# Optimization experiments

Measured on AMD Instinct MI355X. Metric: run time of the kernel, lower is better.

## Reference

```python
import jax, jax.numpy as jnp
import numpy as np

B, L, V, D = 8, 1024, 64, 64  # num_vars == d_model required by the module's g*h broadcast
EPS = 1e-5


def _layer_norm(x, gamma, beta):
    mu = jnp.mean(x, axis=-1, keepdims=True)
    var = jnp.mean(jnp.square(x - mu), axis=-1, keepdims=True)
    return (x - mu) * jax.lax.rsqrt(var + EPS) * gamma + beta


def setup_inputs() -> dict:
    key = jax.random.key(0)
    ks = jax.random.split(key, 20)
    s = 0.05
    inp = {
        'x': jax.random.normal(ks[0], (B, L, V), jnp.float32),
        # per-variable GRN(1, D, D) params, batched over V
        'W1': jax.random.normal(ks[1], (V, D), jnp.float32) * s,   # lin1 weight [in=1 -> D]
        'b1': jax.random.normal(ks[2], (V, D), jnp.float32) * s,
        'W2': jax.random.normal(ks[3], (V, D, D), jnp.float32) * s,
        'b2': jax.random.normal(ks[4], (V, D), jnp.float32) * s,
        'Wg': jax.random.normal(ks[5], (V, D, D), jnp.float32) * s,
        'bg': jax.random.normal(ks[6], (V, D), jnp.float32) * s,
        'Wsk': jax.random.normal(ks[7], (V, D), jnp.float32) * s,  # skip Linear(1, D)
        'bsk': jax.random.normal(ks[8], (V, D), jnp.float32) * s,
        'gamma': jnp.ones((V, D), jnp.float32),
        'beta': jnp.zeros((V, D), jnp.float32),
        # weight_net GRN(V*D, D, V) params
        'Wn1': jax.random.normal(ks[9], (V * D, D), jnp.float32) * s,
        'bn1': jax.random.normal(ks[10], (D,), jnp.float32) * s,
        'Wn2': jax.random.normal(ks[11], (D, D), jnp.float32) * s,
        'bn2': jax.random.normal(ks[12], (D,), jnp.float32) * s,
        'Wng': jax.random.normal(ks[13], (D, V), jnp.float32) * s,
        'bng': jax.random.normal(ks[14], (V,), jnp.float32) * s,
        'Wns': jax.random.normal(ks[15], (V * D, V), jnp.float32) * s,
        'bns': jax.random.normal(ks[16], (V,), jnp.float32) * s,
        'ngamma': jnp.ones((V,), jnp.float32),
        'nbeta': jnp.zeros((V,), jnp.float32),
    }
    return inp


def reference(x, W1, b1, W2, b2, Wg, bg, Wsk, bsk, gamma, beta,
              Wn1, bn1, Wn2, bn2, Wng, bng, Wns, bns, ngamma, nbeta):
    Bx, Lx, Vx = x.shape
    # --- per-variable GRN(1, D, D), batched over the variable axis ---
    h1 = jax.nn.elu(x[..., None] * W1 + b1)                      # [B,L,V,D]
    h2 = jnp.einsum('blvd,vde->blve', h1, W2) + b2               # [B,L,V,D]
    g = jax.nn.sigmoid(jnp.einsum('blvd,vde->blve', h2, Wg) + bg)
    skip = x[..., None] * Wsk + bsk                              # [B,L,V,D]
    stacked = _layer_norm(skip + g * h2, gamma, beta)            # [B,L,V,D]
    # --- weight net GRN(V*D, D, V) + softmax (note: requires V == D) ---
    flat = stacked.reshape(Bx, Lx, Vx * stacked.shape[-1])
    hw = jax.nn.elu(flat @ Wn1 + bn1)                            # [B,L,D]
    hw = hw @ Wn2 + bn2                                          # [B,L,D]
    gw = jax.nn.sigmoid(hw @ Wng + bng)                          # [B,L,V]
    skw = flat @ Wns + bns                                       # [B,L,V]
    weights = jax.nn.softmax(_layer_norm(skw + gw * hw, ngamma, nbeta), axis=-1)
    return jnp.einsum('blv,blvd->bld', weights, stacked)
```

## Files before the change

kernel.cpp:

```cpp
#include <hip/hip_runtime.h>
#include <hip/hip_bf16.h>
#include <math.h>

#define NV 64
#define ND 64
#define NTOK 8192
#define LN_EPS 1e-5f
#define SROW 4096
#define WROW 4096
#define KSPLIT 8
#define KR2 (4096 / KSPLIT)
#define BK 64
#define NKC (KR2 / BK)
#define PROW2 (KSPLIT * 128)

typedef __attribute__((ext_vector_type(8))) short s8v;
typedef __attribute__((ext_vector_type(4))) float f4v;
typedef __attribute__((ext_vector_type(4))) int   i4v;

__device__ __forceinline__ float sigm_f(float x) {
    return __builtin_amdgcn_rcpf(1.f + __expf(-x));
}
__device__ __forceinline__ float elu_f(float x)  { return x > 0.f ? x : (__expf(x) - 1.f); }

__device__ __forceinline__ float bf16_to_f(unsigned short s) {
    union { unsigned int u; float f; } c; c.u = ((unsigned int)s) << 16;
    return c.f;
}
__device__ __forceinline__ unsigned short bf16_rn(float f) {
    union { float f; unsigned int u; } c; c.f = f;
    return (unsigned short)((c.u + 0x8000u) >> 16);
}
__device__ __forceinline__ void async16(const void* g, void* l) {
    __builtin_amdgcn_global_load_lds(
        (const __attribute__((address_space(1))) unsigned int*)g,
        (__attribute__((address_space(3))) unsigned int*)l,
        16, 0, 0);
}

__global__ __launch_bounds__(256) void vsn_prepack(
    const float* __restrict__ W2, const float* __restrict__ Wg,
    const float* __restrict__ Wn1, const float* __restrict__ Wns,
    short* __restrict__ w2b, short* __restrict__ wgb,
    short* __restrict__ wct)
{
    __shared__ float T[64][65];
    const int b = blockIdx.x, t = threadIdx.x;

    if (b < 64) {
        const float* src = W2 + (size_t)b * 4096;
        short* dst = w2b + (size_t)b * 4096;
        #pragma unroll
        for (int pass = 0; pass < 2; ++pass) {
            #pragma unroll
            for (int i = 0; i < 16; ++i) {
                int id = i * 256 + t;
                T[id & 63][id >> 6] = src[id];
            }
            __syncthreads();
            #pragma unroll
            for (int i = 0; i < 16; ++i) {
                int id = i * 256 + t;
                dst[id] = (short)bf16_rn(T[id >> 6][id & 63]);
            }
            __syncthreads();
            src = Wg + (size_t)b * 4096;
            dst = wgb + (size_t)b * 4096;
        }
    } else {
        int tb = b - 64;
        int half = tb >> 6, kt = tb & 63;
        const float* src = (half == 0 ? Wn1 : Wns) + (size_t)(kt * 64) * 64;
        #pragma unroll
        for (int i = 0; i < 16; ++i) {
            int id = i * 256 + t;
            T[id & 63][id >> 6] = src[id];
        }
        __syncthreads();
        #pragma unroll
        for (int i = 0; i < 16; ++i) {
            int id = i * 256 + t;
            int n = id >> 6, r = id & 63;
            wct[(size_t)(half * 64 + n) * WROW + kt * 64 + r] = (short)bf16_rn(T[n][r]);
        }
    }
}

__global__ __launch_bounds__(256) void vsn_stage1(
    const float* __restrict__ x,
    const float* __restrict__ W1, const float* __restrict__ b1,
    const short* __restrict__ w2b, const short* __restrict__ wgb,
    const float* __restrict__ b2, const float* __restrict__ bg,
    const float* __restrict__ Wsk, const float* __restrict__ bsk,
    const float* __restrict__ gamma, const float* __restrict__ beta,
    unsigned short* __restrict__ stb)
{
    const int t = threadIdx.x;
    const int wave = t >> 6, lane = t & 63;
    const int m16 = lane & 15, quad = lane >> 4;
    const int v = blockIdx.y * 4 + wave;

    __shared__ float xs[4][32];
    __shared__ __align__(16) unsigned short h2s[4][32][72];

    float w1k[2][8], b1k[2][8];
    #pragma unroll
    for (int kt = 0; kt < 2; ++kt) {
        *(float4*)&w1k[kt][0] = *(const float4*)(W1 + v * 64 + kt * 32 + quad * 8);
        *(float4*)&w1k[kt][4] = *(const float4*)(W1 + v * 64 + kt * 32 + quad * 8 + 4);
        *(float4*)&b1k[kt][0] = *(const float4*)(b1 + v * 64 + kt * 32 + quad * 8);
        *(float4*)&b1k[kt][4] = *(const float4*)(b1 + v * 64 + kt * 32 + quad * 8 + 4);
    }
    float b2d[4], bgd[4], wskd[4], bskd[4], gamd[4], betd[4];
    #pragma unroll
    for (int ni = 0; ni < 4; ++ni) {
        int d = v * 64 + ni * 16 + m16;
        b2d[ni] = b2[d]; bgd[ni] = bg[d]; wskd[ni] = Wsk[d]; bskd[ni] = bsk[d];
        gamd[ni] = gamma[d]; betd[ni] = beta[d];
    }
    const size_t wb = (size_t)v * 4096;

    for (int tt4 = 0; tt4 < 4; ++tt4) {
        const int tile0 = blockIdx.x * 128 + tt4 * 32;

        if (lane < 32) xs[wave][lane] = x[(size_t)(tile0 + lane) * NV + v];

        s8v a[2][2];
        #pragma unroll
        for (int kt = 0; kt < 2; ++kt)
            #pragma unroll
            for (int mi = 0; mi < 2; ++mi) {
                float xv = xs[wave][mi * 16 + m16];
                float h[8];
                #pragma unroll
                for (int j = 0; j < 8; ++j) h[j] = elu_f(fmaf(xv, w1k[kt][j], b1k[kt][j]));
                i4v av;
                #pragma unroll
                for (int p = 0; p < 4; ++p) {
                    unsigned int u0 = __float_as_uint(h[2 * p]);
                    unsigned int u1 = __float_as_uint(h[2 * p + 1]);
                    av[p] = (int)((u1 & 0xffff0000u) | (u0 >> 16));
                }
                a[mi][kt] = *(s8v*)&av;
            }

        f4v hacc[2][4];
        #pragma unroll
        for (int mi = 0; mi < 2; ++mi)
            #pragma unroll
            for (int ni = 0; ni < 4; ++ni) hacc[mi][ni] = (f4v){0.f, 0.f, 0.f, 0.f};
        #pragma unroll
        for (int ni = 0; ni < 4; ++ni)
            #pragma unroll
            for (int kt = 0; kt < 2; ++kt) {
                s8v bh = *(const s8v*)(w2b + wb + (size_t)(ni * 16 + m16) * 64 + kt * 32 + quad * 8);
                #pragma unroll
                for (int mi = 0; mi < 2; ++mi)
                    hacc[mi][ni] = __builtin_amdgcn_mfma_f32_16x16x32_bf16(a[mi][kt], bh, hacc[mi][ni], 0, 0, 0);
            }
        #pragma unroll
        for (int mi = 0; mi < 2; ++mi)
            #pragma unroll
            for (int ni = 0; ni < 4; ++ni)
                #pragma unroll
                for (int r = 0; r < 4; ++r) hacc[mi][ni][r] += b2d[ni];

        #pragma unroll
        for (int mi = 0; mi < 2; ++mi)
            #pragma unroll
            for (int ni = 0; ni < 4; ++ni)
                #pragma unroll
                for (int r = 0; r < 4; ++r)
                    h2s[wave][mi * 16 + quad * 4 + r][ni * 16 + m16] =
                        (unsigned short)(__float_as_uint(hacc[mi][ni][r]) >> 16);

        s8v c[2][2];
        #pragma unroll
        for (int mi = 0; mi < 2; ++mi)
            #pragma unroll
            for (int kt = 0; kt < 2; ++kt)
                c[mi][kt] = *(const s8v*)&h2s[wave][mi * 16 + m16][kt * 32 + quad * 8];

        f4v gacc[2][4];
        #pragma unroll
        for (int mi = 0; mi < 2; ++mi)
            #pragma unroll
            for (int ni = 0; ni < 4; ++ni) gacc[mi][ni] = (f4v){0.f, 0.f, 0.f, 0.f};
        #pragma unroll
        for (int ni = 0; ni < 4; ++ni)
            #pragma unroll
            for (int kt = 0; kt < 2; ++kt) {
                s8v bh = *(const s8v*)(wgb + wb + (size_t)(ni * 16 + m16) * 64 + kt * 32 + quad * 8);
                #pragma unroll
                for (int mi = 0; mi < 2; ++mi)
                    gacc[mi][ni] = __builtin_amdgcn_mfma_f32_16x16x32_bf16(c[mi][kt], bh, gacc[mi][ni], 0, 0, 0);
            }

        {
            float xtok[2][4];
            #pragma unroll
            for (int mi = 0; mi < 2; ++mi)
                #pragma unroll
                for (int r = 0; r < 4; ++r) xtok[mi][r] = xs[wave][mi * 16 + quad * 4 + r];
            #pragma unroll
            for (int mi = 0; mi < 2; ++mi)
                #pragma unroll
                for (int ni = 0; ni < 4; ++ni)
                    #pragma unroll
                    for (int r = 0; r < 4; ++r) {
                        float g = sigm_f(gacc[mi][ni][r] + bgd[ni]);
                        gacc[mi][ni][r] = fmaf(xtok[mi][r], wskd[ni], bskd[ni]) + g * hacc[mi][ni][r];
                    }
        }

        #pragma unroll
        for (int mi = 0; mi < 2; ++mi)
            #pragma unroll
            for (int r = 0; r < 4; ++r) {
                float s0 = gacc[mi][0][r], s1 = gacc[mi][1][r], s2 = gacc[mi][2][r], s3 = gacc[mi][3][r];
                float sum = s0 + s1 + s2 + s3;
                float sq  = s0 * s0 + s1 * s1 + s2 * s2 + s3 * s3;
                #pragma unroll
                for (int m = 1; m < 16; m <<= 1) { sum += __shfl_xor(sum, m); sq += __shfl_xor(sq, m); }
                float mu  = sum * 0.015625f;
                float var = sq * 0.015625f - mu * mu;
                float rs  = __builtin_amdgcn_rsqf(var + LN_EPS);
                size_t base = (size_t)(tile0 + mi * 16 + quad * 4 + r) * SROW + (size_t)v * 64 + m16;
                #pragma unroll
                for (int ni = 0; ni < 4; ++ni)
                    stb[base + ni * 16] =
                        bf16_rn((gacc[mi][ni][r] - mu) * rs * gamd[ni] + betd[ni]);
            }
    }
}

__global__ __launch_bounds__(512) void vsn_stage2a(
    const unsigned short* __restrict__ stb,
    const short* __restrict__ wct,
    float* __restrict__ part)
{
    const int t = threadIdx.x;
    const int wave = t >> 6, lane = t & 63;
    const int m16 = lane & 15, quad = lane >> 4;
    const int mw = wave & 3, nw = wave >> 2;
    const int tok0 = blockIdx.x * 128;
    const int s = blockIdx.y;
    const int k0 = s * KR2;

    __shared__ __align__(16) unsigned short Al[2][128 * 64];
    __shared__ __align__(16) unsigned short Bl[2][128 * 64];

    const int srow = t >> 3;
    const int schunk = t & 7;

    f4v acc[2][4];
    #pragma unroll
    for (int mi = 0; mi < 2; ++mi)
        #pragma unroll
        for (int nj = 0; nj < 4; ++nj) acc[mi][nj] = (f4v){0.f, 0.f, 0.f, 0.f};

    auto STAGE = [&](int buf, int kc) {
        const int kb = k0 + kc * BK;
        #pragma unroll
        for (int q = 0; q < 2; ++q) {
            const int row = srow + q * 64;
            const int sc = (schunk ^ (row & 7)) * 8;
            async16(stb + (size_t)(tok0 + row) * SROW + kb + sc,
                    &Al[buf][q * 4096 + wave * 512]);
            async16(wct + (size_t)row * WROW + kb + sc,
                    &Bl[buf][q * 4096 + wave * 512]);
        }
    };

    STAGE(0, 0);
    STAGE(1, 1);

    for (int kc = 0; kc < NKC; ++kc) {
        const int buf = kc & 1;
        if (kc + 1 < NKC) asm volatile("s_waitcnt vmcnt(4)" ::: "memory");
        else              asm volatile("s_waitcnt vmcnt(0)" ::: "memory");
        __builtin_amdgcn_s_barrier();
        __builtin_amdgcn_sched_barrier(0);

        #pragma unroll
        for (int ks = 0; ks < 2; ++ks) {
            s8v af[2], bfr[4];
            #pragma unroll
            for (int mi = 0; mi < 2; ++mi) {
                int row = mw * 32 + mi * 16 + m16;
                int ch = ((ks * 4 + quad) ^ (row & 7)) * 8;
                af[mi] = *(const s8v*)&Al[buf][row * 64 + ch];
            }
            #pragma unroll
            for (int nj = 0; nj < 4; ++nj) {
                int row = nw * 64 + nj * 16 + m16;
                int ch = ((ks * 4 + quad) ^ (row & 7)) * 8;
                bfr[nj] = *(const s8v*)&Bl[buf][row * 64 + ch];
            }
            #pragma unroll
            for (int mi = 0; mi < 2; ++mi)
                #pragma unroll
                for (int nj = 0; nj < 4; ++nj)
                    acc[mi][nj] = __builtin_amdgcn_mfma_f32_16x16x32_bf16(af[mi], bfr[nj], acc[mi][nj], 0, 0, 0);
        }

        asm volatile("s_waitcnt lgkmcnt(0)" ::: "memory");
        __builtin_amdgcn_s_barrier();
        __builtin_amdgcn_sched_barrier(0);
        if (kc + 2 < NKC) STAGE(buf, kc + 2);
    }

    #pragma unroll
    for (int mi = 0; mi < 2; ++mi)
        #pragma unroll
        for (int nj = 0; nj < 4; ++nj)
            #pragma unroll
            for (int r = 0; r < 4; ++r)
                part[(size_t)(tok0 + mw * 32 + mi * 16 + quad * 4 + r) * PROW2
                     + s * 128 + nw * 64 + nj * 16 + m16] = acc[mi][nj][r];
}

__global__ __launch_bounds__(256) void vsn_stage2b(
    const unsigned short* __restrict__ stb, const float* __restrict__ part,
    const float* __restrict__ bn1,
    const float* __restrict__ Wn2, const float* __restrict__ bn2,
    const float* __restrict__ Wng, const float* __restrict__ bng,
    const float* __restrict__ bns,
    const float* __restrict__ ngamma, const float* __restrict__ nbeta,
    float* __restrict__ out)
{
    const int t = threadIdx.x;
    const int tok0 = blockIdx.x * 8;
    const int lane = t & 63, wv = t >> 6;

    __shared__ __align__(16) float hw1_s[8][64];
    __shared__ __align__(16) float skw_s[8][64];
    __shared__ __align__(16) float hw2_s[8][64];
    __shared__ float s2_s[8][64];
    __shared__ float w_s[8][64];

    #pragma unroll
    for (int tk = 0; tk < 2; ++tk) {
        int tl = wv * 2 + tk;
        const float* pr = part + (size_t)(tok0 + tl) * PROW2
                        + (lane >> 5) * 128 + (lane & 31) * 4;
        float tv[4] = {0.f, 0.f, 0.f, 0.f};
        #pragma unroll
        for (int i = 0; i < 4; ++i) {
            float4 a = *(const float4*)(pr + i * 256);
            tv[0] += a.x; tv[1] += a.y; tv[2] += a.z; tv[3] += a.w;
        }
        #pragma unroll
        for (int c = 0; c < 4; ++c) tv[c] += __shfl_xor(tv[c], 32);
        if (lane < 16) {
            int j0 = lane * 4;
            float4 bb = *(const float4*)(bn1 + j0);
            hw1_s[tl][j0 + 0] = elu_f(tv[0] + bb.x);
            hw1_s[tl][j0 + 1] = elu_f(tv[1] + bb.y);
            hw1_s[tl][j0 + 2] = elu_f(tv[2] + bb.z);
            hw1_s[tl][j0 + 3] = elu_f(tv[3] + bb.w);
        } else if (lane < 32) {
            int j0 = (lane - 16) * 4;
            float4 bb = *(const float4*)(bns + j0);
            skw_s[tl][j0 + 0] = tv[0] + bb.x;
            skw_s[tl][j0 + 1] = tv[1] + bb.y;
            skw_s[tl][j0 + 2] = tv[2] + bb.z;
            skw_s[tl][j0 + 3] = tv[3] + bb.w;
        }
    }
    __syncthreads();

    #pragma unroll
    for (int i = 0; i < 2; ++i) {
        int oidx = i * 256 + t;
        int tt = oidx >> 6, jj = oidx & 63;
        float acc = bn2[jj];
        #pragma unroll
        for (int k4 = 0; k4 < 16; ++k4) {
            float4 h = *(const float4*)&hw1_s[tt][k4 * 4];
            acc += h.x * Wn2[(k4*4+0)*64+jj] + h.y * Wn2[(k4*4+1)*64+jj]
                 + h.z * Wn2[(k4*4+2)*64+jj] + h.w * Wn2[(k4*4+3)*64+jj];
        }
        hw2_s[tt][jj] = acc;
    }
    __syncthreads();

    #pragma unroll
    for (int i = 0; i < 2; ++i) {
        int oidx = i * 256 + t;
        int tt = oidx >> 6, vv = oidx & 63;
        float acc = bng[vv];
        #pragma unroll
        for (int k4 = 0; k4 < 16; ++k4) {
            float4 h = *(const float4*)&hw2_s[tt][k4 * 4];
            acc += h.x * Wng[(k4*4+0)*64+vv] + h.y * Wng[(k4*4+1)*64+vv]
                 + h.z * Wng[(k4*4+2)*64+vv] + h.w * Wng[(k4*4+3)*64+vv];
        }
        float gw = sigm_f(acc);
        s2_s[tt][vv] = skw_s[tt][vv] + gw * hw2_s[tt][vv];
    }
    __syncthreads();

    const int vloc = lane >> 3, d8 = (lane & 7) * 8;
    s8v r0[8], r1[8];
    {
        const short* s0 = (const short*)stb + (size_t)(tok0 + wv * 2) * SROW + d8;
        const short* s1 = s0 + SROW;
        #pragma unroll
        for (int vc = 0; vc < 8; ++vc) {
            r0[vc] = *(const s8v*)(s0 + (vc * 8 + vloc) * 64);
            r1[vc] = *(const s8v*)(s1 + (vc * 8 + vloc) * 64);
        }
    }

    if (t < 128) {
        int tt = t >> 4, l = t & 15;
        float z[4]; float sum = 0.f, sq = 0.f;
        #pragma unroll
        for (int i = 0; i < 4; ++i) { z[i] = s2_s[tt][l + 16 * i]; sum += z[i]; sq += z[i] * z[i]; }
        #pragma unroll
        for (int m = 1; m < 16; m <<= 1) { sum += __shfl_xor(sum, m); sq += __shfl_xor(sq, m); }
        float mu  = sum * 0.015625f;
        float var = sq * 0.015625f - mu * mu;
        float rs  = __builtin_amdgcn_rsqf(var + LN_EPS);
        float ln[4]; float mx = -1e30f;
        #pragma unroll
        for (int i = 0; i < 4; ++i) {
            ln[i] = (z[i] - mu) * rs * ngamma[l + 16 * i] + nbeta[l + 16 * i];
            mx = fmaxf(mx, ln[i]);
        }
        #pragma unroll
        for (int m = 1; m < 16; m <<= 1) mx = fmaxf(mx, __shfl_xor(mx, m));
        float es = 0.f; float ev[4];
        #pragma unroll
        for (int i = 0; i < 4; ++i) { ev[i] = __expf(ln[i] - mx); es += ev[i]; }
        #pragma unroll
        for (int m = 1; m < 16; m <<= 1) es += __shfl_xor(es, m);
        float inv = __builtin_amdgcn_rcpf(es);
        #pragma unroll
        for (int i = 0; i < 4; ++i) w_s[tt][l + 16 * i] = ev[i] * inv;
    }
    __syncthreads();

    {
        float acc0[8], acc1[8];
        #pragma unroll
        for (int j = 0; j < 8; ++j) { acc0[j] = 0.f; acc1[j] = 0.f; }
        #pragma unroll
        for (int vc = 0; vc < 8; ++vc) {
            int v = vc * 8 + vloc;
            float w0 = w_s[wv * 2][v], w1 = w_s[wv * 2 + 1][v];
            #pragma unroll
            for (int j = 0; j < 8; ++j) {
                acc0[j] = fmaf(w0, bf16_to_f((unsigned short)r0[vc][j]), acc0[j]);
                acc1[j] = fmaf(w1, bf16_to_f((unsigned short)r1[vc][j]), acc1[j]);
            }
        }
        #pragma unroll
        for (int m = 8; m <= 32; m <<= 1)
            #pragma unroll
            for (int j = 0; j < 8; ++j) {
                acc0[j] += __shfl_xor(acc0[j], m);
                acc1[j] += __shfl_xor(acc1[j], m);
            }
        if (lane < 8) {
            float* op = out + (size_t)(tok0 + wv * 2) * 64 + lane * 8;
            *(float4*)op       = make_float4(acc0[0], acc0[1], acc0[2], acc0[3]);
            *(float4*)(op + 4) = make_float4(acc0[4], acc0[5], acc0[6], acc0[7]);
            op += 64;
            *(float4*)op       = make_float4(acc1[0], acc1[1], acc1[2], acc1[3]);
            *(float4*)(op + 4) = make_float4(acc1[4], acc1[5], acc1[6], acc1[7]);
        }
    }
}

extern "C" void kernel_launch(void* const* d_in, const int* in_sizes, int n_in,
                              void* d_out, int out_size, void* d_ws, size_t ws_size,
                              hipStream_t stream) {
    const float* x     = (const float*)d_in[0];
    const float* W1    = (const float*)d_in[1];
    const float* b1    = (const float*)d_in[2];
    const float* W2    = (const float*)d_in[3];
    const float* b2    = (const float*)d_in[4];
    const float* Wg    = (const float*)d_in[5];
    const float* bg    = (const float*)d_in[6];
    const float* Wsk   = (const float*)d_in[7];
    const float* bsk   = (const float*)d_in[8];
    const float* gamma = (const float*)d_in[9];
    const float* beta  = (const float*)d_in[10];
    const float* Wn1   = (const float*)d_in[11];
    const float* bn1   = (const float*)d_in[12];
    const float* Wn2   = (const float*)d_in[13];
    const float* bn2   = (const float*)d_in[14];
    const float* Wng   = (const float*)d_in[15];
    const float* bng   = (const float*)d_in[16];
    const float* Wns   = (const float*)d_in[17];
    const float* bns   = (const float*)d_in[18];
    const float* ngam  = (const float*)d_in[19];
    const float* nbet  = (const float*)d_in[20];

    char* ws = (char*)d_ws;
    unsigned short* stb = (unsigned short*)ws;
    short* wct = (short*)(ws + (64u << 20));
    short* w2b = (short*)(ws + (65u << 20));
    short* wgb = w2b + 262144;
    float* part = (float*)(ws + (66u << 20));
    float* outp = (float*)d_out;

    vsn_prepack<<<dim3(192), 256, 0, stream>>>(W2, Wg, Wn1, Wns, w2b, wgb, wct);
    vsn_stage1<<<dim3(NTOK / 128, 16), 256, 0, stream>>>(
        x, W1, b1, w2b, wgb, b2, bg, Wsk, bsk, gamma, beta, stb);
    vsn_stage2a<<<dim3(NTOK / 128, KSPLIT), 512, 0, stream>>>(stb, wct, part);
    vsn_stage2b<<<dim3(NTOK / 8), 256, 0, stream>>>(
        stb, part, bn1, Wn2, bn2, Wng, bng, bns, ngam, nbet, outp);
}
```

Measured before the change: 185.5 us.

## Fuse weight-net GEMM and epilogue into one kernel without split-K partials

Replaces the split-K stage2a GEMM and the separate stage2b epilogue with a single kernel. Each block handles 32 tokens over the full 4096-wide K, keeps the 128 output columns in registers, and then runs the ELU, Wn2/Wng matvecs, layer norm, softmax and weighted sum in shared memory. This removes the fp32 partial-sum buffer round trip and one launch. Wn2 and Wng are pre-transposed in the prepack kernel so their reads are contiguous. The trade-off is fewer blocks (256) each running a long serial K loop with little MFMA work per wave, and every block re-streams the whole 1 MB wct matrix.

After: 240.2 us. 29.5% more time.

```diff
diff --git a/kernel.cpp b/kernel.cpp
--- a/kernel.cpp
+++ b/kernel.cpp
@@ -8,11 +8,9 @@
 #define LN_EPS 1e-5f
 #define SROW 4096
 #define WROW 4096
-#define KSPLIT 8
-#define KR2 (4096 / KSPLIT)
 #define BK 64
-#define NKC (KR2 / BK)
-#define PROW2 (KSPLIT * 128)
+#define NKC2 (4096 / BK)
+#define MT 32
 
 typedef __attribute__((ext_vector_type(8))) short s8v;
 typedef __attribute__((ext_vector_type(4))) float f4v;
@@ -41,8 +39,10 @@
 __global__ __launch_bounds__(256) void vsn_prepack(
     const float* __restrict__ W2, const float* __restrict__ Wg,
     const float* __restrict__ Wn1, const float* __restrict__ Wns,
+    const float* __restrict__ Wn2, const float* __restrict__ Wng,
     short* __restrict__ w2b, short* __restrict__ wgb,
-    short* __restrict__ wct)
+    short* __restrict__ wct,
+    float* __restrict__ Wn2T, float* __restrict__ WngT)
 {
     __shared__ float T[64][65];
     const int b = blockIdx.x, t = threadIdx.x;
@@ -67,7 +67,7 @@
             src = Wg + (size_t)b * 4096;
             dst = wgb + (size_t)b * 4096;
         }
-    } else {
+    } else if (b < 192) {
         int tb = b - 64;
         int half = tb >> 6, kt = tb & 63;
         const float* src = (half == 0 ? Wn1 : Wns) + (size_t)(kt * 64) * 64;
@@ -82,6 +82,20 @@
             int id = i * 256 + t;
             int n = id >> 6, r = id & 63;
             wct[(size_t)(half * 64 + n) * WROW + kt * 64 + r] = (short)bf16_rn(T[n][r]);
+        }
+    } else {
+        const float* src = (b == 192 ? Wn2 : Wng);
+        float* dst = (b == 192 ? Wn2T : WngT);
+        #pragma unroll
+        for (int i = 0; i < 16; ++i) {
+            int id = i * 256 + t;
+            T[id & 63][id >> 6] = src[id];
+        }
+        __syncthreads();
+        #pragma unroll
+        for (int i = 0; i < 16; ++i) {
+            int id = i * 256 + t;
+            dst[id] = T[id >> 6][id & 63];
         }
     }
 }
@@ -234,190 +248,143 @@
     }
 }
 
-__global__ __launch_bounds__(512) void vsn_stage2a(
+__global__ __launch_bounds__(512) void vsn_stage2(
     const unsigned short* __restrict__ stb,
     const short* __restrict__ wct,
-    float* __restrict__ part)
+    const float* __restrict__ Wn2T, const float* __restrict__ WngT,
+    const float* __restrict__ bn1, const float* __restrict__ bn2,
+    const float* __restrict__ bng, const float* __restrict__ bns,
+    const float* __restrict__ ngamma, const float* __restrict__ nbeta,
+    float* __restrict__ out)
 {
     const int t = threadIdx.x;
     const int wave = t >> 6, lane = t & 63;
     const int m16 = lane & 15, quad = lane >> 4;
-    const int mw = wave & 3, nw = wave >> 2;
-    const int tok0 = blockIdx.x * 128;
-    const int s = blockIdx.y;
-    const int k0 = s * KR2;
-
-    __shared__ __align__(16) unsigned short Al[2][128 * 64];
-    __shared__ __align__(16) unsigned short Bl[2][128 * 64];
-
-    const int srow = t >> 3;
-    const int schunk = t & 7;
-
-    f4v acc[2][4];
-    #pragma unroll
-    for (int mi = 0; mi < 2; ++mi)
-        #pragma unroll
-        for (int nj = 0; nj < 4; ++nj) acc[mi][nj] = (f4v){0.f, 0.f, 0.f, 0.f};
+    const int tok0 = blockIdx.x * MT;
+
+    __shared__ __align__(16) unsigned char smem[43520];
+    unsigned short* Al0 = (unsigned short*)smem;
+    unsigned short* Bl0 = (unsigned short*)(smem + 8192);
+    float* hw1_s = (float*)smem;
+    float* skw_s = (float*)(smem + 8704);
+    float* hw2_s = (float*)(smem + 17408);
+    float* s2_s  = (float*)(smem + 26112);
+    float* w_s   = (float*)(smem + 34816);
+
+    f4v acc[2];
+    acc[0] = (f4v){0.f, 0.f, 0.f, 0.f};
+    acc[1] = (f4v){0.f, 0.f, 0.f, 0.f};
 
     auto STAGE = [&](int buf, int kc) {
-        const int kb = k0 + kc * BK;
+        const int kb = kc * BK;
         #pragma unroll
         for (int q = 0; q < 2; ++q) {
-            const int row = srow + q * 64;
-            const int sc = (schunk ^ (row & 7)) * 8;
+            const int row = wave * 16 + q * 8 + (lane >> 3);
+            const int sc = ((lane & 7) ^ (row & 7)) * 8;
+            async16(wct + (size_t)row * WROW + kb + sc,
+                    &Bl0[buf * 8192 + wave * 1024 + q * 512]);
+        }
+        if (wave < 4) {
+            const int row = wave * 8 + (lane >> 3);
+            const int sc = ((lane & 7) ^ (row & 7)) * 8;
             async16(stb + (size_t)(tok0 + row) * SROW + kb + sc,
-                    &Al[buf][q * 4096 + wave * 512]);
-            async16(wct + (size_t)row * WROW + kb + sc,
-                    &Bl[buf][q * 4096 + wave * 512]);
+                    &Al0[buf * 2048 + wave * 512]);
         }
     };
 
     STAGE(0, 0);
     STAGE(1, 1);
 
-    for (int kc = 0; kc < NKC; ++kc) {
+    for (int kc = 0; kc < NKC2; ++kc) {
         const int buf = kc & 1;
-        if (kc + 1 < NKC) asm volatile("s_waitcnt vmcnt(4)" ::: "memory");
-        else              asm volatile("s_waitcnt vmcnt(0)" ::: "memory");
+        if (kc + 1 < NKC2) {
+            if (wave < 4) asm volatile("s_waitcnt vmcnt(3)" ::: "memory");
+            else          asm volatile("s_waitcnt vmcnt(2)" ::: "memory");
+        } else {
+            asm volatile("s_waitcnt vmcnt(0)" ::: "memory");
+        }
         __builtin_amdgcn_s_barrier();
         __builtin_amdgcn_sched_barrier(0);
 
         #pragma unroll
         for (int ks = 0; ks < 2; ++ks) {
-            s8v af[2], bfr[4];
+            s8v af[2], bf1;
             #pragma unroll
             for (int mi = 0; mi < 2; ++mi) {
-                int row = mw * 32 + mi * 16 + m16;
+                int row = mi * 16 + m16;
                 int ch = ((ks * 4 + quad) ^ (row & 7)) * 8;
-                af[mi] = *(const s8v*)&Al[buf][row * 64 + ch];
-            }
-            #pragma unroll
-            for (int nj = 0; nj < 4; ++nj) {
-                int row = nw * 64 + nj * 16 + m16;
+                af[mi] = *(const s8v*)&Al0[buf * 2048 + row * 64 + ch];
+            }
+            {
+                int row = wave * 16 + m16;
                 int ch = ((ks * 4 + quad) ^ (row & 7)) * 8;
-                bfr[nj] = *(const s8v*)&Bl[buf][row * 64 + ch];
-            }
-            #pragma unroll
-            for (int mi = 0; mi < 2; ++mi)
-                #pragma unroll
-                for (int nj = 0; nj < 4; ++nj)
-                    acc[mi][nj] = __builtin_amdgcn_mfma_f32_16x16x32_bf16(af[mi], bfr[nj], acc[mi][nj], 0, 0, 0);
+                bf1 = *(const s8v*)&Bl0[buf * 8192 + row * 64 + ch];
+            }
+            acc[0] = __builtin_amdgcn_mfma_f32_16x16x32_bf16(af[0], bf1, acc[0], 0, 0, 0);
+            acc[1] = __builtin_amdgcn_mfma_f32_16x16x32_bf16(af[1], bf1, acc[1], 0, 0, 0);
         }
 
         asm volatile("s_waitcnt lgkmcnt(0)" ::: "memory");
         __builtin_amdgcn_s_barrier();
         __builtin_amdgcn_sched_barrier(0);
-        if (kc + 2 < NKC) STAGE(buf, kc + 2);
-    }
+        if (kc + 2 < NKC2) STAGE(buf, kc + 2);
+    }
+
+    if (wave < 4) {
+        const int col = wave * 16 + m16;
+        const float bb = bn1[col];
+        #pragma unroll
+        for (int mi = 0; mi < 2; ++mi)
+            #pragma unroll
+            for (int r = 0; r < 4; ++r)
+                hw1_s[(mi * 16 + quad * 4 + r) * 68 + col] = elu_f(acc[mi][r] + bb);
+    } else {
+        const int col = (wave - 4) * 16 + m16;
+        const float bb = bns[col];
+        #pragma unroll
+        for (int mi = 0; mi < 2; ++mi)
+            #pragma unroll
+            for (int r = 0; r < 4; ++r)
+                skw_s[(mi * 16 + quad * 4 + r) * 68 + col] = acc[mi][r] + bb;
+    }
+    __syncthreads();
 
     #pragma unroll
-    for (int mi = 0; mi < 2; ++mi)
-        #pragma unroll
-        for (int nj = 0; nj < 4; ++nj)
-            #pragma unroll
-            for (int r = 0; r < 4; ++r)
-                part[(size_t)(tok0 + mw * 32 + mi * 16 + quad * 4 + r) * PROW2
-                     + s * 128 + nw * 64 + nj * 16 + m16] = acc[mi][nj][r];
-}
-
-__global__ __launch_bounds__(256) void vsn_stage2b(
-    const unsigned short* __restrict__ stb, const float* __restrict__ part,
-    const float* __restrict__ bn1,
-    const float* __restrict__ Wn2, const float* __restrict__ bn2,
-    const float* __restrict__ Wng, const float* __restrict__ bng,
-    const float* __restrict__ bns,
-    const float* __restrict__ ngamma, const float* __restrict__ nbeta,
-    float* __restrict__ out)
-{
-    const int t = threadIdx.x;
-    const int tok0 = blockIdx.x * 8;
-    const int lane = t & 63, wv = t >> 6;
-
-    __shared__ __align__(16) float hw1_s[8][64];
-    __shared__ __align__(16) float skw_s[8][64];
-    __shared__ __align__(16) float hw2_s[8][64];
-    __shared__ float s2_s[8][64];
-    __shared__ float w_s[8][64];
+    for (int i = 0; i < 4; ++i) {
+        int oidx = i * 512 + t;
+        int tt = oidx >> 6, jj = oidx & 63;
+        float a = bn2[jj];
+        #pragma unroll
+        for (int k4 = 0; k4 < 16; ++k4) {
+            float4 h = *(const float4*)&hw1_s[tt * 68 + k4 * 4];
+            float4 w4 = *(const float4*)(Wn2T + jj * 64 + k4 * 4);
+            a += h.x * w4.x + h.y * w4.y + h.z * w4.z + h.w * w4.w;
+        }
+        hw2_s[tt * 68 + jj] = a;
+    }
+    __syncthreads();
 
     #pragma unroll
-    for (int tk = 0; tk < 2; ++tk) {
-        int tl = wv * 2 + tk;
-        const float* pr = part + (size_t)(tok0 + tl) * PROW2
-                        + (lane >> 5) * 128 + (lane & 31) * 4;
-        float tv[4] = {0.f, 0.f, 0.f, 0.f};
-        #pragma unroll
-        for (int i = 0; i < 4; ++i) {
-            float4 a = *(const float4*)(pr + i * 256);
-            tv[0] += a.x; tv[1] += a.y; tv[2] += a.z; tv[3] += a.w;
-        }
-        #pragma unroll
-        for (int c = 0; c < 4; ++c) tv[c] += __shfl_xor(tv[c], 32);
-        if (lane < 16) {
-            int j0 = lane * 4;
-            float4 bb = *(const float4*)(bn1 + j0);
-            hw1_s[tl][j0 + 0] = elu_f(tv[0] + bb.x);
-            hw1_s[tl][j0 + 1] = elu_f(tv[1] + bb.y);
-            hw1_s[tl][j0 + 2] = elu_f(tv[2] + bb.z);
-            hw1_s[tl][j0 + 3] = elu_f(tv[3] + bb.w);
-        } else if (lane < 32) {
-            int j0 = (lane - 16) * 4;
-            float4 bb = *(const float4*)(bns + j0);
-            skw_s[tl][j0 + 0] = tv[0] + bb.x;
-            skw_s[tl][j0 + 1] = tv[1] + bb.y;
-            skw_s[tl][j0 + 2] = tv[2] + bb.z;
-            skw_s[tl][j0 + 3] = tv[3] + bb.w;
-        }
+    for (int i = 0; i < 4; ++i) {
+        int oidx = i * 512 + t;
+        int tt = oidx >> 6, vv = oidx & 63;
+        float a = bng[vv];
+        #pragma unroll
+        for (int k4 = 0; k4 < 16; ++k4) {
+            float4 h = *(const float4*)&hw2_s[tt * 68 + k4 * 4];
+            float4 w4 = *(const float4*)(WngT + vv * 64 + k4 * 4);
+            a += h.x * w4.x + h.y * w4.y + h.z * w4.z + h.w * w4.w;
+        }
+        float gw = sigm_f(a);
+        s2_s[tt * 68 + vv] = skw_s[tt * 68 + vv] + gw * hw2_s[tt * 68 + vv];
     }
     __syncthreads();
 
-    #pragma unroll
-    for (int i = 0; i < 2; ++i) {
-        int oidx = i * 256 + t;
-        int tt = oidx >> 6, jj = oidx & 63;
-        float acc = bn2[jj];
-        #pragma unroll
-        for (int k4 = 0; k4 < 16; ++k4) {
-            float4 h = *(const float4*)&hw1_s[tt][k4 * 4];
-            acc += h.x * Wn2[(k4*4+0)*64+jj] + h.y * Wn2[(k4*4+1)*64+jj]
-                 + h.z * Wn2[(k4*4+2)*64+jj] + h.w * Wn2[(k4*4+3)*64+jj];
-        }
-        hw2_s[tt][jj] = acc;
-    }
-    __syncthreads();
-
-    #pragma unroll
-    for (int i = 0; i < 2; ++i) {
-        int oidx = i * 256 + t;
-        int tt = oidx >> 6, vv = oidx & 63;
-        float acc = bng[vv];
-        #pragma unroll
-        for (int k4 = 0; k4 < 16; ++k4) {
-            float4 h = *(const float4*)&hw2_s[tt][k4 * 4];
-            acc += h.x * Wng[(k4*4+0)*64+vv] + h.y * Wng[(k4*4+1)*64+vv]
-                 + h.z * Wng[(k4*4+2)*64+vv] + h.w * Wng[(k4*4+3)*64+vv];
-        }
-        float gw = sigm_f(acc);
-        s2_s[tt][vv] = skw_s[tt][vv] + gw * hw2_s[tt][vv];
-    }
-    __syncthreads();
-
-    const int vloc = lane >> 3, d8 = (lane & 7) * 8;
-    s8v r0[8], r1[8];
     {
-        const short* s0 = (const short*)stb + (size_t)(tok0 + wv * 2) * SROW + d8;
-        const short* s1 = s0 + SROW;
-        #pragma unroll
-        for (int vc = 0; vc < 8; ++vc) {
-            r0[vc] = *(const s8v*)(s0 + (vc * 8 + vloc) * 64);
-            r1[vc] = *(const s8v*)(s1 + (vc * 8 + vloc) * 64);
-        }
-    }
-
-    if (t < 128) {
         int tt = t >> 4, l = t & 15;
         float z[4]; float sum = 0.f, sq = 0.f;
         #pragma unroll
-        for (int i = 0; i < 4; ++i) { z[i] = s2_s[tt][l + 16 * i]; sum += z[i]; sq += z[i] * z[i]; }
+        for (int i = 0; i < 4; ++i) { z[i] = s2_s[tt * 68 + l + 16 * i]; sum += z[i]; sq += z[i] * z[i]; }
         #pragma unroll
         for (int m = 1; m < 16; m <<= 1) { sum += __shfl_xor(sum, m); sq += __shfl_xor(sq, m); }
         float mu  = sum * 0.015625f;
@@ -438,38 +405,37 @@
         for (int m = 1; m < 16; m <<= 1) es += __shfl_xor(es, m);
         float inv = __builtin_amdgcn_rcpf(es);
         #pragma unroll
-        for (int i = 0; i < 4; ++i) w_s[tt][l + 16 * i] = ev[i] * inv;
+        for (int i = 0; i < 4; ++i) w_s[tt * 68 + l + 16 * i] = ev[i] * inv;
     }
     __syncthreads();
 
     {
-        float acc0[8], acc1[8];
-        #pragma unroll
-        for (int j = 0; j < 8; ++j) { acc0[j] = 0.f; acc1[j] = 0.f; }
-        #pragma unroll
-        for (int vc = 0; vc < 8; ++vc) {
-            int v = vc * 8 + vloc;
-            float w0 = w_s[wv * 2][v], w1 = w_s[wv * 2 + 1][v];
-            #pragma unroll
-            for (int j = 0; j < 8; ++j) {
-                acc0[j] = fmaf(w0, bf16_to_f((unsigned short)r0[vc][j]), acc0[j]);
-                acc1[j] = fmaf(w1, bf16_to_f((unsigned short)r1[vc][j]), acc1[j]);
-            }
-        }
-        #pragma unroll
-        for (int m = 8; m <= 32; m <<= 1)
-            #pragma unroll
-            for (int j = 0; j < 8; ++j) {
-                acc0[j] += __shfl_xor(acc0[j], m);
-                acc1[j] += __shfl_xor(acc1[j], m);
-            }
-        if (lane < 8) {
-            float* op = out + (size_t)(tok0 + wv * 2) * 64 + lane * 8;
-            *(float4*)op       = make_float4(acc0[0], acc0[1], acc0[2], acc0[3]);
-            *(float4*)(op + 4) = make_float4(acc0[4], acc0[5], acc0[6], acc0[7]);
-            op += 64;
-            *(float4*)op       = make_float4(acc1[0], acc1[1], acc1[2], acc1[3]);
-            *(float4*)(op + 4) = make_float4(acc1[4], acc1[5], acc1[6], acc1[7]);
+        const int vloc = lane >> 3, d8 = (lane & 7) * 8;
+        #pragma unroll
+        for (int tk = 0; tk < 4; ++tk) {
+            const int tl = wave * 4 + tk;
+            const unsigned short* s0 = stb + (size_t)(tok0 + tl) * SROW + d8;
+            float a[8];
+            #pragma unroll
+            for (int j = 0; j < 8; ++j) a[j] = 0.f;
+            #pragma unroll
+            for (int vc = 0; vc < 8; ++vc) {
+                int v = vc * 8 + vloc;
+                float w = w_s[tl * 68 + v];
+                s8v rr = *(const s8v*)(s0 + v * 64);
+                #pragma unroll
+                for (int j = 0; j < 8; ++j)
+                    a[j] = fmaf(w, bf16_to_f((unsigned short)rr[j]), a[j]);
+            }
+            #pragma unroll
+            for (int m = 8; m <= 32; m <<= 1)
+                #pragma unroll
+                for (int j = 0; j < 8; ++j) a[j] += __shfl_xor(a[j], m);
+            if (lane < 8) {
+                float* op = out + (size_t)(tok0 + tl) * 64 + lane * 8;
+                *(float4*)op       = make_float4(a[0], a[1], a[2], a[3]);
+                *(float4*)(op + 4) = make_float4(a[4], a[5], a[6], a[7]);
+            }
         }
     }
 }
@@ -504,13 +470,14 @@
     short* wct = (short*)(ws + (64u << 20));
     short* w2b = (short*)(ws + (65u << 20));
     short* wgb = w2b + 262144;
-    float* part = (float*)(ws + (66u << 20));
+    float* Wn2T = (float*)(ws + (66u << 20));
+    float* WngT = Wn2T + 4096;
     float* outp = (float*)d_out;
 
-    vsn_prepack<<<dim3(192), 256, 0, stream>>>(W2, Wg, Wn1, Wns, w2b, wgb, wct);
+    vsn_prepack<<<dim3(194), 256, 0, stream>>>(W2, Wg, Wn1, Wns, Wn2, Wng,
+                                               w2b, wgb, wct, Wn2T, WngT);
     vsn_stage1<<<dim3(NTOK / 128, 16), 256, 0, stream>>>(
         x, W1, b1, w2b, wgb, b2, bg, Wsk, bsk, gamma, beta, stb);
-    vsn_stage2a<<<dim3(NTOK / 128, KSPLIT), 512, 0, stream>>>(stb, wct, part);
-    vsn_stage2b<<<dim3(NTOK / 8), 256, 0, stream>>>(
-        stb, part, bn1, Wn2, bn2, Wng, bng, bns, ngam, nbet, outp);
-}
+    vsn_stage2<<<dim3(NTOK / MT), 512, 0, stream>>>(
+        stb, wct, Wn2T, WngT, bn1, bn2, bng, bns, ngam, nbet, outp);
+}
```
